# Kernel tuning notes

Hardware: AMD Instinct MI355X
Metric: run time of the kernel (lower is better)

## Reference

```python
import jax, jax.numpy as jnp
import numpy as np

N_NODES = 100000


def gcn_conv(x, src, dst, W, b, n):
    # x: [N, F_in]; src/dst: [E+N] (self-loops already appended)
    h = x @ W  # [N, F_out]
    deg = jax.ops.segment_sum(jnp.ones_like(dst, dtype=h.dtype), dst, num_segments=n)
    dinv = jnp.where(deg > 0, jax.lax.rsqrt(deg), 0.0)
    norm = dinv[src] * dinv[dst]  # [E+N]
    msgs = h[src] * norm[:, None]  # gather + scale
    out = jax.ops.segment_sum(msgs, dst, num_segments=n)  # scatter-add at dst
    return out + b


def setup_inputs() -> dict:
    key = jax.random.key(0)
    k1, k2, k3, ke = jax.random.split(key, 4)
    d = 64
    x = jax.random.normal(k1, (N_NODES, d), dtype=jnp.float32)
    edge_index = jax.random.randint(ke, (2, 1000000), 0, N_NODES, dtype=jnp.int64)
    s = 1.0 / np.sqrt(d)
    W1 = jax.random.normal(k2, (d, d), dtype=jnp.float32) * s
    b1 = jnp.zeros((d,), dtype=jnp.float32)
    W2 = jax.random.normal(k3, (d, d), dtype=jnp.float32) * s
    b2 = jnp.zeros((d,), dtype=jnp.float32)
    return {"x": x, "edge_index": edge_index, "W1": W1, "b1": b1, "W2": W2, "b2": b2}


def reference(x, edge_index, W1, b1, W2, b2):
    n = x.shape[0]
    loops = jnp.arange(n, dtype=edge_index.dtype)
    src = jnp.concatenate([edge_index[0], loops])
    dst = jnp.concatenate([edge_index[1], loops])
    h = gcn_conv(x, src, dst, W1, b1, n)
    h = jax.nn.relu(h)
    out = gcn_conv(h, src, dst, W2, b2, n)
    return out
```

## Files before the change

kernel.cpp:

```cpp
#include <hip/hip_runtime.h>

#define F 64
#define NCH 256

typedef __attribute__((ext_vector_type(8))) short bf16x8;
typedef __attribute__((ext_vector_type(4))) float f32x4;

static __device__ __forceinline__ unsigned short f2bf(float f) {
    unsigned u = __float_as_uint(f);
    return (unsigned short)((u + 0x7fffu + ((u >> 16) & 1u)) >> 16);
}
static __device__ __forceinline__ float bflo(unsigned u) { return __uint_as_float(u << 16); }
static __device__ __forceinline__ float bfhi(unsigned u) { return __uint_as_float(u & 0xffff0000u); }

__global__ __launch_bounds__(256) void k_histprep(const int* __restrict__ dst,
                                                  int* __restrict__ histM,
                                                  const float* __restrict__ W1,
                                                  const float* __restrict__ W2,
                                                  unsigned short* __restrict__ W1t,
                                                  unsigned short* __restrict__ W2t,
                                                  int E, int chunk, int NB) {
    const int t = threadIdx.x;
    if (blockIdx.x >= NCH) {
        int which = blockIdx.x - NCH;
        const float* W = which ? W2 : W1;
        unsigned short* Wt = which ? W2t : W1t;
#pragma unroll
        for (int i = 0; i < 16; ++i) {
            int e = t + i * 256;
            int n = e >> 6, k = e & 63;
            Wt[e] = f2bf(W[k * 64 + n]);
        }
        return;
    }
    extern __shared__ int h[];
    for (int i = t; i < NB; i += 256) h[i] = 0;
    __syncthreads();
    const int lo = blockIdx.x * chunk;
    const int hi = min(E, lo + chunk);
    for (int e = lo + t; e < hi; e += 256) {
        atomicAdd(&h[dst[e] >> 8], 1);
    }
    __syncthreads();
    for (int i = t; i < NB; i += 256) histM[i * NCH + blockIdx.x] = h[i];
}

__global__ __launch_bounds__(256) void s_part(const int* __restrict__ v,
                                              int* __restrict__ part, int M) {
    __shared__ int sd[256];
    const int t = threadIdx.x;
    const int base = blockIdx.x * 1024 + t * 4;
    int s = 0;
    if (base + 3 < M) {
        int4 d = *(const int4*)&v[base];
        s = d.x + d.y + d.z + d.w;
    } else {
#pragma unroll
        for (int j = 0; j < 4; ++j) if (base + j < M) s += v[base + j];
    }
    sd[t] = s;
    __syncthreads();
    for (int off = 128; off > 0; off >>= 1) {
        if (t < off) sd[t] += sd[t + off];
        __syncthreads();
    }
    if (t == 0) part[blockIdx.x] = sd[0];
}

__global__ __launch_bounds__(256) void s_scanp(int* __restrict__ part, int nb) {
    __shared__ int sums[256];
    const int t = threadIdx.x;
    int s = (t < nb) ? part[t] : 0;
    sums[t] = s;
    __syncthreads();
    for (int off = 1; off < 256; off <<= 1) {
        int v = (t >= off) ? sums[t - off] : 0;
        __syncthreads();
        sums[t] += v;
        __syncthreads();
    }
    if (t < nb) part[t] = sums[t] - s;
}

__global__ __launch_bounds__(256) void s_emit(int* __restrict__ v,
                                              const int* __restrict__ part, int M) {
    __shared__ int sums[256];
    const int t = threadIdx.x;
    const int base = blockIdx.x * 1024 + t * 4;
    int d0 = 0, d1 = 0, d2 = 0, d3 = 0;
    if (base + 3 < M) {
        int4 d = *(const int4*)&v[base];
        d0 = d.x; d1 = d.y; d2 = d.z; d3 = d.w;
    } else {
        if (base + 0 < M) d0 = v[base + 0];
        if (base + 1 < M) d1 = v[base + 1];
        if (base + 2 < M) d2 = v[base + 2];
        if (base + 3 < M) d3 = v[base + 3];
    }
    int tot = d0 + d1 + d2 + d3;
    sums[t] = tot;
    __syncthreads();
    for (int off = 1; off < 256; off <<= 1) {
        int x = (t >= off) ? sums[t - off] : 0;
        __syncthreads();
        sums[t] += x;
        __syncthreads();
    }
    int o0 = part[blockIdx.x] + sums[t] - tot;
    int e0 = o0, e1 = o0 + d0, e2 = e1 + d1, e3 = e2 + d2;
    if (base + 3 < M) {
        *(int4*)&v[base] = make_int4(e0, e1, e2, e3);
    } else {
        int ee[4] = {e0, e1, e2, e3};
        for (int j = 0; j < 4; ++j) if (base + j < M) v[base + j] = ee[j];
    }
}

__global__ __launch_bounds__(256) void k_scatter2(const int* __restrict__ src,
                                                  const int* __restrict__ dst,
                                                  const int* __restrict__ scanM,
                                                  int* __restrict__ ebuf,
                                                  int E, int chunk, int NB) {
    extern __shared__ int cur[];
    const int t = threadIdx.x;
    for (int i = t; i < NB; i += 256) cur[i] = scanM[i * NCH + blockIdx.x];
    __syncthreads();
    const int lo = blockIdx.x * chunk;
    const int hi = min(E, lo + chunk);
    for (int e = lo + t; e < hi; e += 256) {
        int s = src[e];
        int d = dst[e];
        int p = atomicAdd(&cur[d >> 8], 1);
        ebuf[p] = s | ((d & 255) << 17);
    }
}

__global__ __launch_bounds__(256) void k_csr(const int* __restrict__ ebuf,
                                             const int* __restrict__ scanM,
                                             int* __restrict__ rowptr,
                                             int* __restrict__ csr,
                                             float* __restrict__ dinv,
                                             int N, int E, int NB) {
    __shared__ int hist[256];
    __shared__ int scn[256];
    __shared__ int cur[256];
    const int t = threadIdx.x;
    const int bkt = blockIdx.x;
    const int beg = scanM[bkt * NCH];
    const int end = (bkt + 1 < NB) ? scanM[(bkt + 1) * NCH] : E;

    hist[t] = 0;
    __syncthreads();
    for (int e = beg + t; e < end; e += 256)
        atomicAdd(&hist[((unsigned)ebuf[e]) >> 17], 1);
    __syncthreads();

    scn[t] = hist[t];
    __syncthreads();
    for (int off = 1; off < 256; off <<= 1) {
        int v = (t >= off) ? scn[t - off] : 0;
        __syncthreads();
        scn[t] += v;
        __syncthreads();
    }

    {
        int excl = scn[t] - hist[t];
        int rp = beg + excl;
        int node = (bkt << 8) + t;
        cur[t] = rp;
        if (node < N) {
            rowptr[node] = rp;
            dinv[node] = rsqrtf((float)(hist[t] + 1));
        }
    }
    if (bkt == NB - 1 && t == 0) rowptr[N] = E;
    __syncthreads();

    for (int e = beg + t; e < end; e += 256) {
        int pk = ebuf[e];
        int p = atomicAdd(&cur[((unsigned)pk) >> 17], 1);
        csr[p] = pk & 0x1FFFF;
    }
}

__global__ __launch_bounds__(256) void k_gemm1(const float* __restrict__ X,
                                               const unsigned short* __restrict__ W1t,
                                               const float* __restrict__ dinv,
                                               unsigned short* __restrict__ hs, int N) {
    __shared__ unsigned short Wl[64 * 72];
    __shared__ unsigned short Xs[64 * 72];
    const int t = threadIdx.x;
    const int row0 = blockIdx.x * 64;

#pragma unroll
    for (int i = 0; i < 2; ++i) {
        int idx = t + i * 256;
        int n = idx >> 3, k = (idx & 7) * 8;
        *(uint4*)&Wl[n * 72 + k] = ((const uint4*)W1t)[idx];
    }
#pragma unroll
    for (int i = 0; i < 4; ++i) {
        int idx = t + i * 256;
        int r = idx >> 4, c = (idx & 15) * 4;
        int gr = row0 + r;
        float4 v = make_float4(0.f, 0.f, 0.f, 0.f);
        if (gr < N) v = *(const float4*)&X[(size_t)gr * F + c];
        unsigned p0 = (unsigned)f2bf(v.x) | ((unsigned)f2bf(v.y) << 16);
        unsigned p1 = (unsigned)f2bf(v.z) | ((unsigned)f2bf(v.w) << 16);
        *(uint2*)&Xs[r * 72 + c] = make_uint2(p0, p1);
    }
    __syncthreads();

    const int w    = t >> 6;
    const int lane = t & 63;
    const int l15  = lane & 15;
    const int quad = lane >> 4;

    bf16x8 bf[4][2];
#pragma unroll
    for (int ct = 0; ct < 4; ++ct)
#pragma unroll
        for (int kc = 0; kc < 2; ++kc)
            bf[ct][kc] = *(const bf16x8*)&Wl[(ct * 16 + l15) * 72 + kc * 32 + quad * 8];

    const int am = w * 16 + l15;
    bf16x8 af0 = *(const bf16x8*)&Xs[am * 72 + quad * 8];
    bf16x8 af1 = *(const bf16x8*)&Xs[am * 72 + 32 + quad * 8];

    f32x4 acc[4];
#pragma unroll
    for (int ct = 0; ct < 4; ++ct) {
        f32x4 z = {0.f, 0.f, 0.f, 0.f};
        z = __builtin_amdgcn_mfma_f32_16x16x32_bf16(af0, bf[ct][0], z, 0, 0, 0);
        z = __builtin_amdgcn_mfma_f32_16x16x32_bf16(af1, bf[ct][1], z, 0, 0, 0);
        acc[ct] = z;
    }

    float dv[4];
#pragma unroll
    for (int r = 0; r < 4; ++r) {
        int row = row0 + w * 16 + quad * 4 + r;
        dv[r] = (row < N) ? dinv[row] : 0.f;
    }
#pragma unroll
    for (int ct = 0; ct < 4; ++ct) {
#pragma unroll
        for (int r = 0; r < 4; ++r) {
            int row = row0 + w * 16 + quad * 4 + r;
            if (row < N)
                hs[(size_t)row * F + ct * 16 + l15] = f2bf(acc[ct][r] * dv[r]);
        }
    }
}

__global__ __launch_bounds__(512) void k_aggmm(const unsigned short* __restrict__ hs1,
                                               const int* __restrict__ rowptr,
                                               const int* __restrict__ csr,
                                               const unsigned short* __restrict__ W2t,
                                               const float* __restrict__ b1,
                                               unsigned short* __restrict__ hs2, int N) {
    __shared__ unsigned short Act[256 * 72];
    __shared__ unsigned short Wl[64 * 72];
    __shared__ float sdv[256];
    const int t = threadIdx.x;
    const int node0 = blockIdx.x << 8;

    {
        int idx = t;
        int n = idx >> 3, k = (idx & 7) * 8;
        *(uint4*)&Wl[n * 72 + k] = ((const uint4*)W2t)[idx];
    }

    const int lane = t & 7;
    const int nsub = t >> 3;
    const uint4* hsb = (const uint4*)hs1;
    float4 bb0 = *(const float4*)&b1[lane * 8];
    float4 bb1 = *(const float4*)&b1[lane * 8 + 4];

#pragma unroll
    for (int it = 0; it < 4; ++it) {
        int local = it * 64 + nsub;
        int node = node0 + local;
        float sc = 0.f;
        unsigned p0 = 0, p1 = 0, p2 = 0, p3 = 0;
        if (node < N) {
            int beg = rowptr[node];
            int end = rowptr[node + 1];
            sc = rsqrtf((float)(end - beg + 1));
            float a0, a1, a2, a3, a4, a5, a6, a7;
            {
                uint4 u = hsb[(size_t)node * 8 + lane];
                a0 = bflo(u.x); a1 = bfhi(u.x);
                a2 = bflo(u.y); a3 = bfhi(u.y);
                a4 = bflo(u.z); a5 = bfhi(u.z);
                a6 = bflo(u.w); a7 = bfhi(u.w);
            }
            for (int base = beg; base < end; base += 16) {
                int i0 = base + lane;
                int i1 = base + 8 + lane;
                int x0 = (i0 < end) ? csr[i0] : 0;
                int x1 = (i1 < end) ? csr[i1] : 0;
                uint4 r[16];
#pragma unroll
                for (int k = 0; k < 8; ++k) {
                    int s = __shfl(x0, k, 8);
                    r[k] = hsb[(size_t)s * 8 + lane];
                }
#pragma unroll
                for (int k = 0; k < 8; ++k) {
                    int s = __shfl(x1, k, 8);
                    r[8 + k] = hsb[(size_t)s * 8 + lane];
                }
                int cnt = min(16, end - base);
#pragma unroll
                for (int k = 0; k < 16; ++k) {
                    if (k < cnt) {
                        uint4 u = r[k];
                        a0 += bflo(u.x); a1 += bfhi(u.x);
                        a2 += bflo(u.y); a3 += bfhi(u.y);
                        a4 += bflo(u.z); a5 += bfhi(u.z);
                        a6 += bflo(u.w); a7 += bfhi(u.w);
                    }
                }
            }
            float o0 = fmaxf(a0 * sc + bb0.x, 0.f), o1 = fmaxf(a1 * sc + bb0.y, 0.f);
            float o2 = fmaxf(a2 * sc + bb0.z, 0.f), o3 = fmaxf(a3 * sc + bb0.w, 0.f);
            float o4 = fmaxf(a4 * sc + bb1.x, 0.f), o5 = fmaxf(a5 * sc + bb1.y, 0.f);
            float o6 = fmaxf(a6 * sc + bb1.z, 0.f), o7 = fmaxf(a7 * sc + bb1.w, 0.f);
            p0 = (unsigned)f2bf(o0) | ((unsigned)f2bf(o1) << 16);
            p1 = (unsigned)f2bf(o2) | ((unsigned)f2bf(o3) << 16);
            p2 = (unsigned)f2bf(o4) | ((unsigned)f2bf(o5) << 16);
            p3 = (unsigned)f2bf(o6) | ((unsigned)f2bf(o7) << 16);
        }
        *(uint4*)&Act[local * 72 + lane * 8] = make_uint4(p0, p1, p2, p3);
        if (lane == 0) sdv[local] = sc;
    }
    __syncthreads();

    const int w    = t >> 6;
    const int l    = t & 63;
    const int l15  = l & 15;
    const int quad = l >> 4;

    bf16x8 bf[4][2];
#pragma unroll
    for (int nt = 0; nt < 4; ++nt)
#pragma unroll
        for (int kc = 0; kc < 2; ++kc)
            bf[nt][kc] = *(const bf16x8*)&Wl[(nt * 16 + l15) * 72 + kc * 32 + quad * 8];

#pragma unroll
    for (int mt = 0; mt < 2; ++mt) {
        int m0 = w * 32 + mt * 16;
        bf16x8 af0 = *(const bf16x8*)&Act[(m0 + l15) * 72 + quad * 8];
        bf16x8 af1 = *(const bf16x8*)&Act[(m0 + l15) * 72 + 32 + quad * 8];
#pragma unroll
        for (int nt = 0; nt < 4; ++nt) {
            f32x4 z = {0.f, 0.f, 0.f, 0.f};
            z = __builtin_amdgcn_mfma_f32_16x16x32_bf16(af0, bf[nt][0], z, 0, 0, 0);
            z = __builtin_amdgcn_mfma_f32_16x16x32_bf16(af1, bf[nt][1], z, 0, 0, 0);
#pragma unroll
            for (int r = 0; r < 4; ++r) {
                int row = m0 + quad * 4 + r;
                int node = node0 + row;
                if (node < N)
                    hs2[((size_t)nt * N + node) * 16 + l15] = f2bf(z[r] * sdv[row]);
            }
        }
    }
}

__global__ __launch_bounds__(256) void k_agg2(const unsigned short* __restrict__ hs2,
                                              const int* __restrict__ rowptr,
                                              const int* __restrict__ csr,
                                              const float* __restrict__ dinv,
                                              const float* __restrict__ b,
                                              float* __restrict__ out, int N) {
    const int slice = blockIdx.x & 3;
    const int chunk = blockIdx.x >> 2;
    const int t = threadIdx.x;
    const int node = chunk * 128 + (t >> 1);
    const int lane = t & 1;
    if (node >= N) return;
    const int beg = rowptr[node];
    const int end = rowptr[node + 1];
    const unsigned short* hp = hs2 + (size_t)slice * N * 16;

    float a[16];
#pragma unroll
    for (int j = 0; j < 16; ++j) a[j] = 0.f;

    for (int e = beg + lane; e < end; e += 2) {
        int s = csr[e];
        const uint4* p = (const uint4*)(hp + (size_t)s * 16);
        uint4 u0 = p[0];
        uint4 u1 = p[1];
        a[0] += bflo(u0.x); a[1] += bfhi(u0.x);
        a[2] += bflo(u0.y); a[3] += bfhi(u0.y);
        a[4] += bflo(u0.z); a[5] += bfhi(u0.z);
        a[6] += bflo(u0.w); a[7] += bfhi(u0.w);
        a[8]  += bflo(u1.x); a[9]  += bfhi(u1.x);
        a[10] += bflo(u1.y); a[11] += bfhi(u1.y);
        a[12] += bflo(u1.z); a[13] += bfhi(u1.z);
        a[14] += bflo(u1.w); a[15] += bfhi(u1.w);
    }
#pragma unroll
    for (int j = 0; j < 16; ++j) a[j] += __shfl_xor(a[j], 1, 2);

    const float sc = dinv[node];
    const int j0 = lane * 8;
    uint4 sv = *(const uint4*)(hp + (size_t)node * 16 + j0);
    float s0 = bflo(sv.x), s1 = bfhi(sv.x), s2 = bflo(sv.y), s3 = bfhi(sv.y);
    float s4 = bflo(sv.z), s5 = bfhi(sv.z), s6 = bflo(sv.w), s7 = bfhi(sv.w);
    float4 bb0 = *(const float4*)&b[slice * 16 + j0];
    float4 bb1 = *(const float4*)&b[slice * 16 + j0 + 4];
    float4 o0 = make_float4((a[j0 + 0] + s0) * sc + bb0.x,
                            (a[j0 + 1] + s1) * sc + bb0.y,
                            (a[j0 + 2] + s2) * sc + bb0.z,
                            (a[j0 + 3] + s3) * sc + bb0.w);
    float4 o1 = make_float4((a[j0 + 4] + s4) * sc + bb1.x,
                            (a[j0 + 5] + s5) * sc + bb1.y,
                            (a[j0 + 6] + s6) * sc + bb1.z,
                            (a[j0 + 7] + s7) * sc + bb1.w);
    float* op = &out[(size_t)node * F + slice * 16 + j0];
    *(float4*)op = o0;
    *(float4*)(op + 4) = o1;
}

extern "C" void kernel_launch(void* const* d_in, const int* in_sizes, int n_in,
                              void* d_out, int out_size, void* d_ws, size_t ws_size,
                              hipStream_t stream) {
    const float* x  = (const float*)d_in[0];
    const int*   ei = (const int*)d_in[1];
    const float* W1 = (const float*)d_in[2];
    const float* b1 = (const float*)d_in[3];
    const float* W2 = (const float*)d_in[4];
    const float* b2 = (const float*)d_in[5];
    float* out = (float*)d_out;

    const int N = in_sizes[0] / F;
    const int E = in_sizes[1] / 2;
    const int* src = ei;
    const int* dst = ei + E;

    const int NB = (N + 255) >> 8;
    const int chunk = (E + NCH - 1) / NCH;
    const int M  = NB * NCH;
    const int Mp = ((M + 1023) / 1024) * 1024;
    const int nb2 = Mp / 1024;

    char* ws = (char*)d_ws;
    size_t a = 0;
    unsigned short* W1t = (unsigned short*)(ws + a); a += (4096 * 2 + 255) & ~(size_t)255;
    unsigned short* W2t = (unsigned short*)(ws + a); a += (4096 * 2 + 255) & ~(size_t)255;
    float* dinv   = (float*)(ws + a); a += ((size_t)N * 4 + 255) & ~(size_t)255;
    int*   part2  = (int*)(ws + a);   a += ((size_t)nb2 * 4 + 255) & ~(size_t)255;
    int*   rowptr = (int*)(ws + a);   a += ((size_t)(N + 1) * 4 + 255) & ~(size_t)255;
    int*   histM  = (int*)(ws + a);   a += ((size_t)Mp * 4 + 255) & ~(size_t)255;
    int*   ebuf   = (int*)(ws + a);   a += ((size_t)E * 4 + 255) & ~(size_t)255;
    int*   csr    = (int*)(ws + a);   a += ((size_t)E * 4 + 255) & ~(size_t)255;
    unsigned short* hs1 = (unsigned short*)(ws + a); a += ((size_t)N * F * 2 + 255) & ~(size_t)255;
    unsigned short* hs2 = (unsigned short*)(ws + a);

    const size_t ldsNB = (size_t)NB * 4;
    const int gGemm = (N + 63) / 64;
    const int gAgg2 = ((N + 127) / 128) * 4;

    k_histprep<<<NCH + 2, 256, ldsNB, stream>>>(dst, histM, W1, W2, W1t, W2t, E, chunk, NB);
    s_part<<<nb2, 256, 0, stream>>>(histM, part2, M);
    s_scanp<<<1, 256, 0, stream>>>(part2, nb2);
    s_emit<<<nb2, 256, 0, stream>>>(histM, part2, M);
    k_scatter2<<<NCH, 256, ldsNB, stream>>>(src, dst, histM, ebuf, E, chunk, NB);
    k_csr<<<NB, 256, 0, stream>>>(ebuf, histM, rowptr, csr, dinv, N, E, NB);

    k_gemm1<<<gGemm, 256, 0, stream>>>(x, W1t, dinv, hs1, N);
    k_aggmm<<<NB, 512, 0, stream>>>(hs1, rowptr, csr, W2t, b1, hs2, N);
    k_agg2<<<gAgg2, 256, 0, stream>>>(hs2, rowptr, csr, dinv, b2, out, N);
}
```

Before: 190.3 us.

## Use four lanes per node in final aggregation with prefetched neighbor indices

The second-layer aggregation kernel now gives each node four threads instead of two, doubling the grid. Each lane prefetches CSR indices two iterations ahead and processes two neighbors per iteration to expose more memory-level parallelism. A butterfly shuffle reduction leaves each lane owning four output features, so each lane writes one float4. The cost is more threads per node, a larger grid, and extra shuffle work for low-degree nodes.

```diff
diff --git a/kernel.cpp b/kernel.cpp
--- a/kernel.cpp
+++ b/kernel.cpp
@@ -380,8 +380,8 @@
     const int slice = blockIdx.x & 3;
     const int chunk = blockIdx.x >> 2;
     const int t = threadIdx.x;
-    const int node = chunk * 128 + (t >> 1);
-    const int lane = t & 1;
+    const int node = chunk * 64 + (t >> 2);
+    const int lane = t & 3;
     if (node >= N) return;
     const int beg = rowptr[node];
     const int end = rowptr[node + 1];
@@ -391,41 +391,68 @@
 #pragma unroll
     for (int j = 0; j < 16; ++j) a[j] = 0.f;
 
-    for (int e = beg + lane; e < end; e += 2) {
-        int s = csr[e];
-        const uint4* p = (const uint4*)(hp + (size_t)s * 16);
-        uint4 u0 = p[0];
-        uint4 u1 = p[1];
-        a[0] += bflo(u0.x); a[1] += bfhi(u0.x);
-        a[2] += bflo(u0.y); a[3] += bfhi(u0.y);
-        a[4] += bflo(u0.z); a[5] += bfhi(u0.z);
-        a[6] += bflo(u0.w); a[7] += bfhi(u0.w);
-        a[8]  += bflo(u1.x); a[9]  += bfhi(u1.x);
-        a[10] += bflo(u1.y); a[11] += bfhi(u1.y);
-        a[12] += bflo(u1.z); a[13] += bfhi(u1.z);
-        a[14] += bflo(u1.w); a[15] += bfhi(u1.w);
-    }
-#pragma unroll
-    for (int j = 0; j < 16; ++j) a[j] += __shfl_xor(a[j], 1, 2);
+    int e = beg + lane;
+    int i0 = (e < end) ? csr[e] : -1;
+    int i1 = (e + 4 < end) ? csr[e + 4] : -1;
+    while (i0 >= 0) {
+        int i2 = (e + 8  < end) ? csr[e + 8]  : -1;
+        int i3 = (e + 12 < end) ? csr[e + 12] : -1;
+        {
+            const uint4* p = (const uint4*)(hp + (size_t)i0 * 16);
+            uint4 u0 = p[0];
+            uint4 u1 = p[1];
+            a[0] += bflo(u0.x); a[1] += bfhi(u0.x);
+            a[2] += bflo(u0.y); a[3] += bfhi(u0.y);
+            a[4] += bflo(u0.z); a[5] += bfhi(u0.z);
+            a[6] += bflo(u0.w); a[7] += bfhi(u0.w);
+            a[8]  += bflo(u1.x); a[9]  += bfhi(u1.x);
+            a[10] += bflo(u1.y); a[11] += bfhi(u1.y);
+            a[12] += bflo(u1.z); a[13] += bfhi(u1.z);
+            a[14] += bflo(u1.w); a[15] += bfhi(u1.w);
+        }
+        if (i1 >= 0) {
+            const uint4* p = (const uint4*)(hp + (size_t)i1 * 16);
+            uint4 u0 = p[0];
+            uint4 u1 = p[1];
+            a[0] += bflo(u0.x); a[1] += bfhi(u0.x);
+            a[2] += bflo(u0.y); a[3] += bfhi(u0.y);
+            a[4] += bflo(u0.z); a[5] += bfhi(u0.z);
+            a[6] += bflo(u0.w); a[7] += bfhi(u0.w);
+            a[8]  += bflo(u1.x); a[9]  += bfhi(u1.x);
+            a[10] += bflo(u1.y); a[11] += bfhi(u1.y);
+            a[12] += bflo(u1.z); a[13] += bfhi(u1.z);
+            a[14] += bflo(u1.w); a[15] += bfhi(u1.w);
+        }
+        i0 = i2;
+        i1 = i3;
+        e += 8;
+    }
+
+    float h[8];
+#pragma unroll
+    for (int k = 0; k < 8; ++k) {
+        float lo = a[k]     + __shfl_xor(a[k], 2, 4);
+        float hi = a[k + 8] + __shfl_xor(a[k + 8], 2, 4);
+        h[k] = (lane & 2) ? hi : lo;
+    }
+    float v[4];
+#pragma unroll
+    for (int k = 0; k < 4; ++k) {
+        float lo = h[k]     + __shfl_xor(h[k], 1, 4);
+        float hi = h[k + 4] + __shfl_xor(h[k + 4], 1, 4);
+        v[k] = (lane & 1) ? hi : lo;
+    }
 
     const float sc = dinv[node];
-    const int j0 = lane * 8;
-    uint4 sv = *(const uint4*)(hp + (size_t)node * 16 + j0);
+    const int j0 = lane * 4;
+    uint2 sv = *(const uint2*)(hp + (size_t)node * 16 + j0);
     float s0 = bflo(sv.x), s1 = bfhi(sv.x), s2 = bflo(sv.y), s3 = bfhi(sv.y);
-    float s4 = bflo(sv.z), s5 = bfhi(sv.z), s6 = bflo(sv.w), s7 = bfhi(sv.w);
-    float4 bb0 = *(const float4*)&b[slice * 16 + j0];
-    float4 bb1 = *(const float4*)&b[slice * 16 + j0 + 4];
-    float4 o0 = make_float4((a[j0 + 0] + s0) * sc + bb0.x,
-                            (a[j0 + 1] + s1) * sc + bb0.y,
-                            (a[j0 + 2] + s2) * sc + bb0.z,
-                            (a[j0 + 3] + s3) * sc + bb0.w);
-    float4 o1 = make_float4((a[j0 + 4] + s4) * sc + bb1.x,
-                            (a[j0 + 5] + s5) * sc + bb1.y,
-                            (a[j0 + 6] + s6) * sc + bb1.z,
-                            (a[j0 + 7] + s7) * sc + bb1.w);
-    float* op = &out[(size_t)node * F + slice * 16 + j0];
-    *(float4*)op = o0;
-    *(float4*)(op + 4) = o1;
+    float4 bb = *(const float4*)&b[slice * 16 + j0];
+    float4 o = make_float4((v[0] + s0) * sc + bb.x,
+                           (v[1] + s1) * sc + bb.y,
+                           (v[2] + s2) * sc + bb.z,
+                           (v[3] + s3) * sc + bb.w);
+    *(float4*)&out[(size_t)node * F + slice * 16 + j0] = o;
 }
 
 extern "C" void kernel_launch(void* const* d_in, const int* in_sizes, int n_in,
@@ -465,7 +492,7 @@
 
     const size_t ldsNB = (size_t)NB * 4;
     const int gGemm = (N + 63) / 64;
-    const int gAgg2 = ((N + 127) / 128) * 4;
+    const int gAgg2 = ((N + 63) / 64) * 4;
 
     k_histprep<<<NCH + 2, 256, ldsNB, stream>>>(dst, histM, W1, W2, W1t, W2t, E, chunk, NB);
     s_part<<<nb2, 256, 0, stream>>>(histM, part2, M);
```

New measurement: 181.8 us. 4.5% less time.
